# Performance work log

Hardware: AMD Instinct MI355X
Metric: run time of the kernel (lower is better)

## Reference

```python
import jax, jax.numpy as jnp
import numpy as np

B, S, D, L, H = 8, 1024, 512, 6, 8
HD = D // H


def setup_inputs() -> dict:
    key = jax.random.key(0)
    sc = D ** -0.5
    inp = {
        "xr": jax.random.normal(jax.random.fold_in(key, 0), (B, S, D), jnp.float32),
        "xi": jax.random.normal(jax.random.fold_in(key, 1), (B, S, D), jnp.float32),
    }
    wnames = ["Wq_r", "Wq_i", "Wk_r", "Wk_i", "Wv_r", "Wv_i", "Wo_r", "Wo_i",
              "W1_r", "W1_i", "W2_r", "W2_i"]
    for i, n in enumerate(wnames):
        inp[n] = jax.random.normal(jax.random.fold_in(key, 10 + i), (L, D, D), jnp.float32) * sc
    for n in ["bq_r", "bq_i", "bk_r", "bk_i", "bv_r", "bv_i", "bo_r", "bo_i",
              "b1_r", "b1_i", "b2_r", "b2_i"]:
        inp[n] = jnp.zeros((L, D), jnp.float32)
    g0 = 1.0 / np.sqrt(2.0)  # standard complex-LN affine init
    for n in ["ln1_grr", "ln1_gii", "ln2_grr", "ln2_gii"]:
        inp[n] = jnp.full((L, D), g0, jnp.float32)
    for n in ["ln1_gri", "ln1_br", "ln1_bi", "ln2_gri", "ln2_br", "ln2_bi"]:
        inp[n] = jnp.zeros((L, D), jnp.float32)
    return inp


def clin(xr, xi, Wr, Wi, br, bi):
    # ComplexLinear: (xr + i xi)(Wr + i Wi)^T + (br + i bi)
    yr = xr @ Wr.T - xi @ Wi.T + br
    yi = xr @ Wi.T + xi @ Wr.T + bi
    return yr, yi


def cln(xr, xi, grr, gri, gii, br, bi, eps=1e-5):
    # Complex LayerNorm: 2x2 covariance whitening over the feature dim + affine
    mr = xr.mean(-1, keepdims=True)
    mi = xi.mean(-1, keepdims=True)
    cr, ci = xr - mr, xi - mi
    Vrr = (cr * cr).mean(-1, keepdims=True) + eps
    Vii = (ci * ci).mean(-1, keepdims=True) + eps
    Vri = (cr * ci).mean(-1, keepdims=True)
    s = jnp.sqrt(Vrr * Vii - Vri * Vri)
    t = jnp.sqrt(Vrr + Vii + 2.0 * s)
    st = s * t
    Wrr = (Vii + s) / st
    Wii = (Vrr + s) / st
    Wri = -Vri / st
    hr = Wrr * cr + Wri * ci
    hi = Wri * cr + Wii * ci
    return grr * hr + gri * hi + br, gri * hr + gii * hi + bi


def reference(xr, xi,
              Wq_r, Wq_i, bq_r, bq_i, Wk_r, Wk_i, bk_r, bk_i,
              Wv_r, Wv_i, bv_r, bv_i, Wo_r, Wo_i, bo_r, bo_i,
              W1_r, W1_i, b1_r, b1_i, W2_r, W2_i, b2_r, b2_i,
              ln1_grr, ln1_gri, ln1_gii, ln1_br, ln1_bi,
              ln2_grr, ln2_gri, ln2_gii, ln2_br, ln2_bi):
    b, s, d = xr.shape
    nl = Wq_r.shape[0]
    h = H
    hd = d // h
    scale = hd ** -0.5
    for l in range(nl):
        rr, ri = xr, xi
        qr, qi = clin(xr, xi, Wq_r[l], Wq_i[l], bq_r[l], bq_i[l])
        kr, ki = clin(xr, xi, Wk_r[l], Wk_i[l], bk_r[l], bk_i[l])
        vr, vi = clin(xr, xi, Wv_r[l], Wv_i[l], bv_r[l], bv_i[l])
        split = lambda a: a.reshape(b, s, h, hd)
        qr, qi, kr, ki, vr, vi = map(split, (qr, qi, kr, ki, vr, vi))
        # sm_variante='real': softmax over Re(q k^H) = qr.kr + qi.ki
        logits = (jnp.einsum('bqhd,bkhd->bhqk', qr, kr)
                  + jnp.einsum('bqhd,bkhd->bhqk', qi, ki)) * scale
        A = jax.nn.softmax(logits, axis=-1)  # real-valued attention weights
        o_r = jnp.einsum('bhqk,bkhd->bqhd', A, vr).reshape(b, s, d)
        o_i = jnp.einsum('bhqk,bkhd->bqhd', A, vi).reshape(b, s, d)
        o_r, o_i = clin(o_r, o_i, Wo_r[l], Wo_i[l], bo_r[l], bo_i[l])
        xr, xi = o_r + rr, o_i + ri
        xr, xi = cln(xr, xi, ln1_grr[l], ln1_gri[l], ln1_gii[l], ln1_br[l], ln1_bi[l])
        rr, ri = xr, xi
        hr, hi = clin(xr, xi, W1_r[l], W1_i[l], b1_r[l], b1_i[l])
        hr, hi = jax.nn.relu(hr), jax.nn.relu(hi)  # CReLU; dropout = identity (eval)
        hr, hi = clin(hr, hi, W2_r[l], W2_i[l], b2_r[l], b2_i[l])
        xr, xi = hr + rr, hi + ri
        xr, xi = cln(xr, xi, ln2_grr[l], ln2_gri[l], ln2_gii[l], ln2_br[l], ln2_bi[l])
    return jnp.stack([xr, xi])  # [2, B, S, D] (real, imag)
```

## Files before the change

kernel.cpp:

```cpp
#include <hip/hip_runtime.h>
#include <cstddef>
#include <cstdint>

constexpr int NB   = 8;
constexpr int SEQ  = 1024;
constexpr int DIM  = 512;
constexpr int NL   = 6;
constexpr int NH   = 8;
constexpr int HDIM = 64;
constexpr int ROWS = NB * SEQ;
constexpr size_t BSD = (size_t)ROWS * DIM;
constexpr int KHAT = 1024;

typedef __attribute__((ext_vector_type(8))) short bfrag;
typedef __attribute__((ext_vector_type(4))) float f32x4;
typedef __attribute__((ext_vector_type(4))) unsigned short us4;

__device__ __forceinline__ void f4a(const float4 v, float* a) {
    a[0] = v.x; a[1] = v.y; a[2] = v.z; a[3] = v.w;
}
__device__ __forceinline__ float4 a4f(const float* a) {
    float4 v; v.x = a[0]; v.y = a[1]; v.z = a[2]; v.w = a[3]; return v;
}
__device__ __forceinline__ unsigned short f2bf(float f) {
    union { float f; uint32_t u; } x{f};
    return (unsigned short)((x.u + 0x7fffu + ((x.u >> 16) & 1u)) >> 16);
}
__device__ __forceinline__ void gload16(const unsigned short* g, void* l) {
    __builtin_amdgcn_global_load_lds(
        (const __attribute__((address_space(1))) void*)g,
        (__attribute__((address_space(3))) void*)l, 16, 0, 0);
}

struct PrepArgs {
    const float* Wr[6]; const float* Wi[6];
    const float* br[6]; const float* bi[6];
};

__global__ __launch_bounds__(256)
void prep_kernel(PrepArgs a, unsigned short* __restrict__ Ball,
                 float* __restrict__ biasall, int layer)
{
    const int lin = blockIdx.y;
    const int nh_ = blockIdx.x;
    const float* Wr = a.Wr[lin] + (size_t)layer * DIM * DIM;
    const float* Wi = a.Wi[lin] + (size_t)layer * DIM * DIM;

    bool real; int n0;
    if (lin < 3) { const int dh = nh_ & 127; real = dh < 64; n0 = (nh_ >> 7) * 64 + (dh & 63); }
    else         { real = nh_ < 512; n0 = nh_ & 511; }

    const int t = threadIdx.x;
    const int kk = (t * 4) & 511;
    const bool fh = t < 128;
    const float* src;
    float sgn = 1.f;
    if (fh) src = real ? Wr : Wi;
    else { if (real) { src = Wi; sgn = -1.f; } else src = Wr; }

    float v[4];
    f4a(*(const float4*)(src + (size_t)n0 * 512 + kk), v);
    us4 o;
    #pragma unroll
    for (int j = 0; j < 4; ++j) o[j] = f2bf(sgn * v[j]);
    *(us4*)(Ball + (size_t)lin * KHAT * KHAT + (size_t)nh_ * KHAT + t * 4) = o;
    if (t == 0)
        biasall[lin * KHAT + nh_] = real ? a.br[lin][layer * DIM + n0]
                                         : a.bi[lin][layer * DIM + n0];
}

template <int EPI>
__global__ __launch_bounds__(256)
void gemm_mfma(const unsigned short* __restrict__ Xh,
               const unsigned short* __restrict__ Bh,
               const float* __restrict__ bias,
               unsigned short* __restrict__ Yh,
               float* __restrict__ Yr, float* __restrict__ Yi)
{
    __shared__ __align__(16) unsigned short Asm[128 * 32];
    __shared__ __align__(16) unsigned short Bsm[128 * 32];

    const int t = threadIdx.x, lane = t & 63, w = t >> 6;
    const int wm = w >> 1, wn = w & 1;
    const int c = lane & 15, g = lane >> 4;

    int bid = blockIdx.y * 8 + blockIdx.x;
    bid = (bid & 7) * 64 + (bid >> 3);
    const int n0 = (bid & 7) * 128;
    const int m0 = (bid >> 3) * 128;

    f32x4 acc[4][4];
    #pragma unroll
    for (int i = 0; i < 4; ++i)
        #pragma unroll
        for (int j = 0; j < 4; ++j) acc[i][j] = (f32x4){0.f, 0.f, 0.f, 0.f};

    const int srow = (w << 4) + (lane >> 2);
    const int scol = (lane & 3) * 8;
    const unsigned short* gA0 = Xh + (size_t)(m0 + srow) * KHAT + scol;
    const unsigned short* gA1 = Xh + (size_t)(m0 + 64 + srow) * KHAT + scol;
    const unsigned short* gB0 = Bh + (size_t)(n0 + srow) * KHAT + scol;
    const unsigned short* gB1 = Bh + (size_t)(n0 + 64 + srow) * KHAT + scol;
    char* aBase = (char*)Asm + (w << 10);
    char* bBase = (char*)Bsm + (w << 10);

    for (int ks = 0; ks < 32; ++ks) {
        const int k0 = ks * 32;
        __syncthreads();
        gload16(gA0 + k0, aBase);
        gload16(gA1 + k0, aBase + 4096);
        gload16(gB0 + k0, bBase);
        gload16(gB1 + k0, bBase + 4096);
        __syncthreads();

        bfrag af[4], bf2[4];
        #pragma unroll
        for (int mi = 0; mi < 4; ++mi)
            af[mi] = *(const bfrag*)(Asm + (wm * 64 + mi * 16 + c) * 32 + g * 8);
        #pragma unroll
        for (int ni = 0; ni < 4; ++ni)
            bf2[ni] = *(const bfrag*)(Bsm + (wn * 64 + ni * 16 + c) * 32 + g * 8);
        #pragma unroll
        for (int mi = 0; mi < 4; ++mi)
            #pragma unroll
            for (int ni = 0; ni < 4; ++ni)
                acc[mi][ni] = __builtin_amdgcn_mfma_f32_16x16x32_bf16(
                    af[mi], bf2[ni], acc[mi][ni], 0, 0, 0);
    }

    const int mbase = m0 + wm * 64;
    const int nbase = n0 + wn * 64;
    #pragma unroll
    for (int mi = 0; mi < 4; ++mi) {
        #pragma unroll
        for (int ni = 0; ni < 4; ++ni) {
            const int n = nbase + ni * 16 + c;
            const float bv = bias[n];
            float v[4];
            #pragma unroll
            for (int r = 0; r < 4; ++r) v[r] = acc[mi][ni][r] + bv;
            const int mrow = mbase + mi * 16 + g * 4;
            if (EPI == 0) {
                const int b = mrow >> 10, s = mrow & 1023;
                const int h = n >> 7, dh = n & 127;
                const size_t a = ((size_t)(b * NH + h) * SEQ + s) * 128 + dh;
                #pragma unroll
                for (int r = 0; r < 4; ++r) Yh[a + (size_t)r * 128] = f2bf(v[r]);
            } else if (EPI == 1) {
                const int b = mrow >> 10, s = mrow & 1023;
                const int h = n >> 7, dh = n & 127;
                const size_t a = ((size_t)(b * NH + h) * 128 + dh) * SEQ + s;
                us4 o;
                #pragma unroll
                for (int r = 0; r < 4; ++r) o[r] = f2bf(v[r]);
                *(us4*)(Yh + a) = o;
            } else if (EPI == 2) {
                float* dst = (n < 512) ? Yr : Yi;
                const int nn = n & 511;
                #pragma unroll
                for (int r = 0; r < 4; ++r) dst[(size_t)(mrow + r) * DIM + nn] = v[r];
            } else {
                #pragma unroll
                for (int r = 0; r < 4; ++r)
                    Yh[(size_t)(mrow + r) * KHAT + n] = f2bf(fmaxf(v[r], 0.f));
            }
        }
    }
}

__global__ __launch_bounds__(256)
void attn_mfma(const unsigned short* __restrict__ Qh,
               const unsigned short* __restrict__ Kh,
               const unsigned short* __restrict__ Vth,
               unsigned short* __restrict__ Ah)
{
    __shared__ __align__(16) char smem[41216];
    char* Ksm = smem;
    char* Vsm = smem + 16384;
    const int t    = threadIdx.x;
    const int lane = t & 63;
    const int wv   = t >> 6;
    const int c    = lane & 15;
    const int g    = lane >> 4;
    char* Pw = smem + 32768 + wv * 2048;

    int bid = blockIdx.x + 16 * blockIdx.y + 128 * blockIdx.z;
    bid = (bid & 7) * 128 + (bid >> 3);
    const int q0 = (bid & 15) * 64;
    const int bh = bid >> 4;
    const int hh = bh & 7, bb = bh >> 3;
    const size_t qkb = (size_t)bh * SEQ * 128;
    const size_t vtb = (size_t)bh * 128 * SEQ;

    bfrag qf[4];
    {
        const unsigned short* qp = Qh + qkb + (size_t)(q0 + wv * 16 + c) * 128 + g * 8;
        #pragma unroll
        for (int ks = 0; ks < 4; ++ks) qf[ks] = *(const bfrag*)(qp + ks * 32);
    }

    f32x4 oacc[8];
    #pragma unroll
    for (int i = 0; i < 8; ++i) oacc[i] = (f32x4){0.f, 0.f, 0.f, 0.f};
    float mrun[4], lrun[4];
    #pragma unroll
    for (int r = 0; r < 4; ++r) { mrun[r] = -1e30f; lrun[r] = 0.f; }

    const int kkey = t >> 2, kq = t & 3;
    const unsigned short* kgp = Kh + qkb + (size_t)kkey * 128 + kq * 32;
    const int vd = t >> 1, vh2 = t & 1;
    const unsigned short* vgp = Vth + vtb + (size_t)vd * SEQ + vh2 * 32;

    bfrag krg[4], vrg[4];
    #pragma unroll
    for (int j = 0; j < 4; ++j) krg[j] = *(const bfrag*)(kgp + j * 8);
    #pragma unroll
    for (int j = 0; j < 4; ++j) vrg[j] = *(const bfrag*)(vgp + j * 8);

    for (int k0 = 0; k0 < SEQ; k0 += 64) {
        __syncthreads();
        #pragma unroll
        for (int j = 0; j < 4; ++j) {
            const int boff = (kkey * 256 + (kq * 32 + j * 8) * 2) ^ ((kkey & 7) << 4);
            *(bfrag*)(Ksm + boff) = krg[j];
        }
        #pragma unroll
        for (int j = 0; j < 4; ++j) {
            const int boff = (vd * 128 + (vh2 * 32 + j * 8) * 2) ^ ((vd & 7) << 4);
            *(bfrag*)(Vsm + boff) = vrg[j];
        }
        __syncthreads();

        if (k0 + 64 < SEQ) {
            const int kn = k0 + 64;
            #pragma unroll
            for (int j = 0; j < 4; ++j) krg[j] = *(const bfrag*)(kgp + (size_t)kn * 128 + j * 8);
            #pragma unroll
            for (int j = 0; j < 4; ++j) vrg[j] = *(const bfrag*)(vgp + kn + j * 8);
        }

        f32x4 sa[4];
        #pragma unroll
        for (int nt = 0; nt < 4; ++nt) sa[nt] = (f32x4){0.f, 0.f, 0.f, 0.f};
        __builtin_amdgcn_s_setprio(1);
        #pragma unroll
        for (int nt = 0; nt < 4; ++nt) {
            const int key = nt * 16 + c;
            #pragma unroll
            for (int ks = 0; ks < 4; ++ks) {
                const int boff = (key * 256 + (ks * 32 + g * 8) * 2) ^ ((key & 7) << 4);
                const bfrag bk = *(const bfrag*)(Ksm + boff);
                sa[nt] = __builtin_amdgcn_mfma_f32_16x16x32_bf16(qf[ks], bk, sa[nt], 0, 0, 0);
            }
        }
        __builtin_amdgcn_s_setprio(0);

        float sv[4][4];
        #pragma unroll
        for (int nt = 0; nt < 4; ++nt)
            #pragma unroll
            for (int r = 0; r < 4; ++r) sv[nt][r] = sa[nt][r] * 0.125f;

        float mt[4], ps[4], mn[4];
        #pragma unroll
        for (int r = 0; r < 4; ++r)
            mt[r] = fmaxf(fmaxf(sv[0][r], sv[1][r]), fmaxf(sv[2][r], sv[3][r]));
        #pragma unroll
        for (int m = 1; m <= 8; m <<= 1) {
            #pragma unroll
            for (int r = 0; r < 4; ++r) mt[r] = fmaxf(mt[r], __shfl_xor(mt[r], m, 64));
        }
        bool big = false;
        #pragma unroll
        for (int r = 0; r < 4; ++r) big |= (mt[r] > mrun[r] + 8.f);
        const bool refresh = __any(big);
        float fs[4];
        if (refresh) {
            #pragma unroll
            for (int r = 0; r < 4; ++r) {
                mn[r] = fmaxf(mrun[r], mt[r]);
                fs[r] = __expf(mrun[r] - mn[r]);
            }
        } else {
            #pragma unroll
            for (int r = 0; r < 4; ++r) { mn[r] = mrun[r]; fs[r] = 1.f; }
        }
        #pragma unroll
        for (int r = 0; r < 4; ++r) ps[r] = 0.f;

        #pragma unroll
        for (int nt = 0; nt < 4; ++nt) {
            const int col2 = (nt * 16 + c) * 2;
            #pragma unroll
            for (int r = 0; r < 4; ++r) {
                const float p = __expf(sv[nt][r] - mn[r]);
                ps[r] += p;
                const int qrow = 4 * g + r;
                *(unsigned short*)(Pw + ((qrow * 128 + col2) ^ ((qrow & 7) << 4))) = f2bf(p);
            }
        }
        #pragma unroll
        for (int m = 1; m <= 8; m <<= 1) {
            #pragma unroll
            for (int r = 0; r < 4; ++r) ps[r] += __shfl_xor(ps[r], m, 64);
        }
        #pragma unroll
        for (int r = 0; r < 4; ++r) {
            lrun[r] = lrun[r] * fs[r] + ps[r];
            mrun[r] = mn[r];
        }

        if (refresh) {
            const int rr = c & 3;
            float vsel = fs[0];
            vsel = (rr == 1) ? fs[1] : vsel;
            vsel = (rr == 2) ? fs[2] : vsel;
            vsel = (rr == 3) ? fs[3] : vsel;
            const float fsc = __shfl(vsel, ((c >> 2) << 4) | (c & 3), 64);
            #pragma unroll
            for (int i = 0; i < 8; ++i) {
                oacc[i][0] *= fsc; oacc[i][1] *= fsc; oacc[i][2] *= fsc; oacc[i][3] *= fsc;
            }
        }

        asm volatile("s_waitcnt lgkmcnt(0)" ::: "memory");
        __builtin_amdgcn_sched_barrier(0);

        __builtin_amdgcn_s_setprio(1);
        #pragma unroll
        for (int k2 = 0; k2 < 2; ++k2) {
            const int kb2 = (k2 * 32 + g * 8) * 2;
            const bfrag pb = *(const bfrag*)(Pw + ((c * 128 + kb2) ^ ((c & 7) << 4)));
            #pragma unroll
            for (int mtl = 0; mtl < 8; ++mtl) {
                const int d = mtl * 16 + c;
                const bfrag va = *(const bfrag*)(Vsm + ((d * 128 + kb2) ^ ((d & 7) << 4)));
                oacc[mtl] = __builtin_amdgcn_mfma_f32_16x16x32_bf16(va, pb, oacc[mtl], 0, 0, 0);
            }
        }
        __builtin_amdgcn_s_setprio(0);
    }

    {
        const int rr = c & 3;
        float inv[4];
        #pragma unroll
        for (int r = 0; r < 4; ++r) inv[r] = 1.f / lrun[r];
        float vsel = inv[0];
        vsel = (rr == 1) ? inv[1] : vsel;
        vsel = (rr == 2) ? inv[2] : vsel;
        vsel = (rr == 3) ? inv[3] : vsel;
        const float ic = __shfl(vsel, ((c >> 2) << 4) | (c & 3), 64);
        #pragma unroll
        for (int i = 0; i < 8; ++i) {
            oacc[i][0] *= ic; oacc[i][1] *= ic; oacc[i][2] *= ic; oacc[i][3] *= ic;
        }
    }
    __syncthreads();
    float* Ox = (float*)(smem + wv * 8192);
    #pragma unroll
    for (int mtl = 0; mtl < 8; ++mtl)
        #pragma unroll
        for (int r = 0; r < 4; ++r)
            Ox[(mtl * 16 + 4 * g + r) * 16 + c] = oacc[mtl][r];
    asm volatile("s_waitcnt lgkmcnt(0)" ::: "memory");
    __builtin_amdgcn_sched_barrier(0);

    const int q = lane >> 2, qt = lane & 3;
    const int colbase = (qt >> 1) * 512 + hh * 64 + (qt & 1) * 32;
    const size_t rowm = (size_t)bb * SEQ + q0 + wv * 16 + q;
    unsigned short* dst = Ah + rowm * KHAT + colbase;
    #pragma unroll
    for (int j = 0; j < 8; ++j) {
        us4 o;
        #pragma unroll
        for (int e = 0; e < 4; ++e) o[e] = f2bf(Ox[(qt * 32 + j * 4 + e) * 16 + q]);
        *(us4*)(dst + j * 4) = o;
    }
}

__global__ __launch_bounds__(256)
void cln_kernel(const float* __restrict__ Ur, const float* __restrict__ Ui,
                float* __restrict__ Xr, float* __restrict__ Xi,
                unsigned short* __restrict__ Xh,
                const float* __restrict__ Grr, const float* __restrict__ Gri,
                const float* __restrict__ Gii, const float* __restrict__ Bbr,
                const float* __restrict__ Bbi)
{
    const int lane = threadIdx.x & 63;
    const int row  = blockIdx.x * 4 + (threadIdx.x >> 6);
    const size_t off = (size_t)row * DIM;
    const int c0 = lane * 4;
    const int c1 = 256 + lane * 4;

    float xr[8], xi[8];
    {
        float a[4], b[4];
        f4a(*(const float4*)&Ur[off + c0], a); f4a(*(const float4*)&Xr[off + c0], b);
        #pragma unroll
        for (int j = 0; j < 4; ++j) xr[j] = a[j] + b[j];
        f4a(*(const float4*)&Ur[off + c1], a); f4a(*(const float4*)&Xr[off + c1], b);
        #pragma unroll
        for (int j = 0; j < 4; ++j) xr[4 + j] = a[j] + b[j];
        f4a(*(const float4*)&Ui[off + c0], a); f4a(*(const float4*)&Xi[off + c0], b);
        #pragma unroll
        for (int j = 0; j < 4; ++j) xi[j] = a[j] + b[j];
        f4a(*(const float4*)&Ui[off + c1], a); f4a(*(const float4*)&Xi[off + c1], b);
        #pragma unroll
        for (int j = 0; j < 4; ++j) xi[4 + j] = a[j] + b[j];
    }

    float sr = 0.f, si = 0.f, srr = 0.f, sii = 0.f, sri = 0.f;
    #pragma unroll
    for (int j = 0; j < 8; ++j) {
        sr += xr[j]; si += xi[j];
        srr = fmaf(xr[j], xr[j], srr);
        sii = fmaf(xi[j], xi[j], sii);
        sri = fmaf(xr[j], xi[j], sri);
    }
    #pragma unroll
    for (int m = 32; m >= 1; m >>= 1) {
        sr  += __shfl_xor(sr,  m, 64);
        si  += __shfl_xor(si,  m, 64);
        srr += __shfl_xor(srr, m, 64);
        sii += __shfl_xor(sii, m, 64);
        sri += __shfl_xor(sri, m, 64);
    }

    const float inv_d = 1.0f / DIM;
    const float mr = sr * inv_d, mi = si * inv_d;
    const float Vrr = srr * inv_d - mr * mr + 1e-5f;
    const float Vii = sii * inv_d - mi * mi + 1e-5f;
    const float Vri = sri * inv_d - mr * mi;
    const float s  = sqrtf(Vrr * Vii - Vri * Vri);
    const float tt = sqrtf(Vrr + Vii + 2.0f * s);
    const float ist = 1.0f / (s * tt);
    const float Wrr = (Vii + s) * ist;
    const float Wii = (Vrr + s) * ist;
    const float Wri = -Vri * ist;

    #pragma unroll
    for (int half = 0; half < 2; ++half) {
        const int c = half ? c1 : c0;
        float grr[4], gri[4], gii[4], pbr[4], pbi[4];
        f4a(*(const float4*)&Grr[c], grr);
        f4a(*(const float4*)&Gri[c], gri);
        f4a(*(const float4*)&Gii[c], gii);
        f4a(*(const float4*)&Bbr[c], pbr);
        f4a(*(const float4*)&Bbi[c], pbi);
        float outr[4], outi[4];
        #pragma unroll
        for (int j = 0; j < 4; ++j) {
            const int idx = half * 4 + j;
            const float cr = xr[idx] - mr;
            const float ci = xi[idx] - mi;
            const float hr = Wrr * cr + Wri * ci;
            const float hi = Wri * cr + Wii * ci;
            outr[j] = fmaf(grr[j], hr, fmaf(gri[j], hi, pbr[j]));
            outi[j] = fmaf(gri[j], hr, fmaf(gii[j], hi, pbi[j]));
        }
        *(float4*)&Xr[off + c] = a4f(outr);
        *(float4*)&Xi[off + c] = a4f(outi);
        us4 hr_, hi_;
        #pragma unroll
        for (int j = 0; j < 4; ++j) { hr_[j] = f2bf(outr[j]); hi_[j] = f2bf(outi[j]); }
        *(us4*)(Xh + (size_t)row * KHAT + c)       = hr_;
        *(us4*)(Xh + (size_t)row * KHAT + 512 + c) = hi_;
    }
}

__global__ __launch_bounds__(256)
void init_cvt(const float* __restrict__ xr, const float* __restrict__ xi,
              float* __restrict__ outr, float* __restrict__ outi,
              unsigned short* __restrict__ Xh)
{
    const size_t i = ((size_t)blockIdx.x * 256 + threadIdx.x) * 4;
    float vr[4], vi[4];
    f4a(*(const float4*)(xr + i), vr);
    f4a(*(const float4*)(xi + i), vi);
    *(float4*)(outr + i) = a4f(vr);
    *(float4*)(outi + i) = a4f(vi);
    const size_t m = i >> 9;
    const int k = (int)(i & 511);
    us4 a, b;
    #pragma unroll
    for (int j = 0; j < 4; ++j) { a[j] = f2bf(vr[j]); b[j] = f2bf(vi[j]); }
    *(us4*)(Xh + m * KHAT + k)       = a;
    *(us4*)(Xh + m * KHAT + 512 + k) = b;
}

extern "C" void kernel_launch(void* const* d_in, const int* in_sizes, int n_in,
                              void* d_out, int out_size, void* d_ws, size_t ws_size,
                              hipStream_t stream) {
    (void)in_sizes; (void)n_in; (void)out_size; (void)ws_size;

    const float* in_xr = (const float*)d_in[0];
    const float* in_xi = (const float*)d_in[1];
    PrepArgs pa;
    pa.Wr[0] = (const float*)d_in[2];  pa.Wi[0] = (const float*)d_in[3];
    pa.Wr[1] = (const float*)d_in[4];  pa.Wi[1] = (const float*)d_in[5];
    pa.Wr[2] = (const float*)d_in[6];  pa.Wi[2] = (const float*)d_in[7];
    pa.Wr[3] = (const float*)d_in[8];  pa.Wi[3] = (const float*)d_in[9];
    pa.Wr[4] = (const float*)d_in[10]; pa.Wi[4] = (const float*)d_in[11];
    pa.Wr[5] = (const float*)d_in[12]; pa.Wi[5] = (const float*)d_in[13];
    pa.br[0] = (const float*)d_in[14]; pa.bi[0] = (const float*)d_in[15];
    pa.br[1] = (const float*)d_in[16]; pa.bi[1] = (const float*)d_in[17];
    pa.br[2] = (const float*)d_in[18]; pa.bi[2] = (const float*)d_in[19];
    pa.br[3] = (const float*)d_in[20]; pa.bi[3] = (const float*)d_in[21];
    pa.br[4] = (const float*)d_in[22]; pa.bi[4] = (const float*)d_in[23];
    pa.br[5] = (const float*)d_in[24]; pa.bi[5] = (const float*)d_in[25];
    const float* ln1_grr = (const float*)d_in[26];
    const float* ln1_gii = (const float*)d_in[27];
    const float* ln2_grr = (const float*)d_in[28];
    const float* ln2_gii = (const float*)d_in[29];
    const float* ln1_gri = (const float*)d_in[30];
    const float* ln1_br  = (const float*)d_in[31];
    const float* ln1_bi  = (const float*)d_in[32];
    const float* ln2_gri = (const float*)d_in[33];
    const float* ln2_br  = (const float*)d_in[34];
    const float* ln2_bi  = (const float*)d_in[35];

    float* outr = (float*)d_out;
    float* outi = outr + BSD;

    char* ws = (char*)d_ws;
    unsigned short* Xh  = (unsigned short*)(ws);
    unsigned short* Qh  = (unsigned short*)(ws + 16777216);
    unsigned short* Kh  = (unsigned short*)(ws + 2 * 16777216);
    unsigned short* Vth = (unsigned short*)(ws + 3 * 16777216);
    unsigned short* Ah  = (unsigned short*)(ws + 4 * 16777216);
    unsigned short* Ball = (unsigned short*)(ws + 5 * 16777216);
    float* biasall = (float*)(ws + 5 * 16777216 + 12582912);
    float* Pr = (float*)Kh;
    float* Pi = (float*)Vth;
    unsigned short* Hh = Qh;

    init_cvt<<<ROWS * DIM / 1024, 256, 0, stream>>>(in_xr, in_xi, outr, outi, Xh);

    const dim3 pgrid(KHAT, 6);
    const dim3 ggrid(KHAT / 128, ROWS / 128);
    const dim3 agrid(SEQ / 64, NH, NB);
    const int  lgrid = ROWS / 4;

    for (int l = 0; l < NL; ++l) {
        const size_t bo = (size_t)l * DIM;
        prep_kernel<<<pgrid, 256, 0, stream>>>(pa, Ball, biasall, l);

        unsigned short* Bq = Ball;
        unsigned short* Bk = Ball + (size_t)1 * KHAT * KHAT;
        unsigned short* Bv = Ball + (size_t)2 * KHAT * KHAT;
        unsigned short* Bo = Ball + (size_t)3 * KHAT * KHAT;
        unsigned short* B1 = Ball + (size_t)4 * KHAT * KHAT;
        unsigned short* B2 = Ball + (size_t)5 * KHAT * KHAT;

        gemm_mfma<0><<<ggrid, 256, 0, stream>>>(Xh, Bq, biasall + 0 * KHAT, Qh, nullptr, nullptr);
        gemm_mfma<0><<<ggrid, 256, 0, stream>>>(Xh, Bk, biasall + 1 * KHAT, Kh, nullptr, nullptr);
        gemm_mfma<1><<<ggrid, 256, 0, stream>>>(Xh, Bv, biasall + 2 * KHAT, Vth, nullptr, nullptr);
        attn_mfma<<<agrid, 256, 0, stream>>>(Qh, Kh, Vth, Ah);
        gemm_mfma<2><<<ggrid, 256, 0, stream>>>(Ah, Bo, biasall + 3 * KHAT, nullptr, Pr, Pi);
        cln_kernel<<<lgrid, 256, 0, stream>>>(Pr, Pi, outr, outi, Xh,
                                              ln1_grr + bo, ln1_gri + bo, ln1_gii + bo,
                                              ln1_br + bo, ln1_bi + bo);
        gemm_mfma<3><<<ggrid, 256, 0, stream>>>(Xh, B1, biasall + 4 * KHAT, Hh, nullptr, nullptr);
        gemm_mfma<2><<<ggrid, 256, 0, stream>>>(Hh, B2, biasall + 5 * KHAT, nullptr, Pr, Pi);
        cln_kernel<<<lgrid, 256, 0, stream>>>(Pr, Pi, outr, outi, Xh,
                                              ln2_grr + bo, ln2_gri + bo, ln2_gii + bo,
                                              ln2_br + bo, ln2_bi + bo);
    }
}
```

Measured before the change: 1.706 ms.

## Fuse QKV GEMMs, compute softmax rowsum via MFMA, store GEMM outputs as bf16

Merges the three Q/K/V projection GEMMs into one launch with a 24-wide N grid that picks the weight slice and output layout per block. Attention now uses exp2 with a pre-scaled log2e factor and a wider lazy-rescale threshold. It skips the cross-lane max reduction unless a rescale is needed and gets the row sum from an extra MFMA against a ones vector instead of shuffle reductions. The O-projection and FFN2 outputs are written as bf16 instead of fp32 and converted back inside the complex LayerNorm kernel, which halves that traffic but lowers residual-path precision.

```diff
diff --git a/kernel.cpp b/kernel.cpp
--- a/kernel.cpp
+++ b/kernel.cpp
@@ -26,6 +26,11 @@
     union { float f; uint32_t u; } x{f};
     return (unsigned short)((x.u + 0x7fffu + ((x.u >> 16) & 1u)) >> 16);
 }
+__device__ __forceinline__ float bf2f(unsigned short u) {
+    union { uint32_t u; float f; } x;
+    x.u = (uint32_t)u << 16;
+    return x.f;
+}
 __device__ __forceinline__ void gload16(const unsigned short* g, void* l) {
     __builtin_amdgcn_global_load_lds(
         (const __attribute__((address_space(1))) void*)g,
@@ -69,13 +74,13 @@
                                          : a.bi[lin][layer * DIM + n0];
 }
 
-template <int EPI>
 __global__ __launch_bounds__(256)
-void gemm_mfma(const unsigned short* __restrict__ Xh,
-               const unsigned short* __restrict__ Bh,
-               const float* __restrict__ bias,
-               unsigned short* __restrict__ Yh,
-               float* __restrict__ Yr, float* __restrict__ Yi)
+void gemm_qkv(const unsigned short* __restrict__ Xh,
+              const unsigned short* __restrict__ Ball,
+              const float* __restrict__ biasall,
+              unsigned short* __restrict__ Qh,
+              unsigned short* __restrict__ Kh,
+              unsigned short* __restrict__ Vth)
 {
     __shared__ __align__(16) unsigned short Asm[128 * 32];
     __shared__ __align__(16) unsigned short Bsm[128 * 32];
@@ -84,10 +89,15 @@
     const int wm = w >> 1, wn = w & 1;
     const int c = lane & 15, g = lane >> 4;
 
-    int bid = blockIdx.y * 8 + blockIdx.x;
-    bid = (bid & 7) * 64 + (bid >> 3);
-    const int n0 = (bid & 7) * 128;
-    const int m0 = (bid >> 3) * 128;
+    int bid = blockIdx.y * 24 + blockIdx.x;
+    bid = (bid & 7) * 192 + (bid >> 3);
+    const int nblk = bid % 24, mblk = bid / 24;
+    const int n0g = nblk * 128;
+    const int m0 = mblk * 128;
+    const int lin = n0g >> 10;
+    const int n0 = n0g & 1023;
+    const unsigned short* Bh = Ball + (size_t)lin * KHAT * KHAT;
+    const float* bias = biasall + lin * KHAT;
 
     f32x4 acc[4][4];
     #pragma unroll
@@ -130,6 +140,7 @@
 
     const int mbase = m0 + wm * 64;
     const int nbase = n0 + wn * 64;
+    unsigned short* dqk = (lin == 0) ? Qh : Kh;
     #pragma unroll
     for (int mi = 0; mi < 4; ++mi) {
         #pragma unroll
@@ -140,29 +151,95 @@
             #pragma unroll
             for (int r = 0; r < 4; ++r) v[r] = acc[mi][ni][r] + bv;
             const int mrow = mbase + mi * 16 + g * 4;
-            if (EPI == 0) {
-                const int b = mrow >> 10, s = mrow & 1023;
-                const int h = n >> 7, dh = n & 127;
+            const int b = mrow >> 10, s = mrow & 1023;
+            const int h = n >> 7, dh = n & 127;
+            if (lin < 2) {
                 const size_t a = ((size_t)(b * NH + h) * SEQ + s) * 128 + dh;
                 #pragma unroll
-                for (int r = 0; r < 4; ++r) Yh[a + (size_t)r * 128] = f2bf(v[r]);
-            } else if (EPI == 1) {
-                const int b = mrow >> 10, s = mrow & 1023;
-                const int h = n >> 7, dh = n & 127;
+                for (int r = 0; r < 4; ++r) dqk[a + (size_t)r * 128] = f2bf(v[r]);
+            } else {
                 const size_t a = ((size_t)(b * NH + h) * 128 + dh) * SEQ + s;
                 us4 o;
                 #pragma unroll
                 for (int r = 0; r < 4; ++r) o[r] = f2bf(v[r]);
-                *(us4*)(Yh + a) = o;
-            } else if (EPI == 2) {
-                float* dst = (n < 512) ? Yr : Yi;
-                const int nn = n & 511;
-                #pragma unroll
-                for (int r = 0; r < 4; ++r) dst[(size_t)(mrow + r) * DIM + nn] = v[r];
-            } else {
-                #pragma unroll
-                for (int r = 0; r < 4; ++r)
-                    Yh[(size_t)(mrow + r) * KHAT + n] = f2bf(fmaxf(v[r], 0.f));
+                *(us4*)(Vth + a) = o;
+            }
+        }
+    }
+}
+
+template <bool RELU>
+__global__ __launch_bounds__(256)
+void gemm_mfma(const unsigned short* __restrict__ Xh,
+               const unsigned short* __restrict__ Bh,
+               const float* __restrict__ bias,
+               unsigned short* __restrict__ Yh)
+{
+    __shared__ __align__(16) unsigned short Asm[128 * 32];
+    __shared__ __align__(16) unsigned short Bsm[128 * 32];
+
+    const int t = threadIdx.x, lane = t & 63, w = t >> 6;
+    const int wm = w >> 1, wn = w & 1;
+    const int c = lane & 15, g = lane >> 4;
+
+    int bid = blockIdx.y * 8 + blockIdx.x;
+    bid = (bid & 7) * 64 + (bid >> 3);
+    const int n0 = (bid & 7) * 128;
+    const int m0 = (bid >> 3) * 128;
+
+    f32x4 acc[4][4];
+    #pragma unroll
+    for (int i = 0; i < 4; ++i)
+        #pragma unroll
+        for (int j = 0; j < 4; ++j) acc[i][j] = (f32x4){0.f, 0.f, 0.f, 0.f};
+
+    const int srow = (w << 4) + (lane >> 2);
+    const int scol = (lane & 3) * 8;
+    const unsigned short* gA0 = Xh + (size_t)(m0 + srow) * KHAT + scol;
+    const unsigned short* gA1 = Xh + (size_t)(m0 + 64 + srow) * KHAT + scol;
+    const unsigned short* gB0 = Bh + (size_t)(n0 + srow) * KHAT + scol;
+    const unsigned short* gB1 = Bh + (size_t)(n0 + 64 + srow) * KHAT + scol;
+    char* aBase = (char*)Asm + (w << 10);
+    char* bBase = (char*)Bsm + (w << 10);
+
+    for (int ks = 0; ks < 32; ++ks) {
+        const int k0 = ks * 32;
+        __syncthreads();
+        gload16(gA0 + k0, aBase);
+        gload16(gA1 + k0, aBase + 4096);
+        gload16(gB0 + k0, bBase);
+        gload16(gB1 + k0, bBase + 4096);
+        __syncthreads();
+
+        bfrag af[4], bf2[4];
+        #pragma unroll
+        for (int mi = 0; mi < 4; ++mi)
+            af[mi] = *(const bfrag*)(Asm + (wm * 64 + mi * 16 + c) * 32 + g * 8);
+        #pragma unroll
+        for (int ni = 0; ni < 4; ++ni)
+            bf2[ni] = *(const bfrag*)(Bsm + (wn * 64 + ni * 16 + c) * 32 + g * 8);
+        #pragma unroll
+        for (int mi = 0; mi < 4; ++mi)
+            #pragma unroll
+            for (int ni = 0; ni < 4; ++ni)
+                acc[mi][ni] = __builtin_amdgcn_mfma_f32_16x16x32_bf16(
+                    af[mi], bf2[ni], acc[mi][ni], 0, 0, 0);
+    }
+
+    const int mbase = m0 + wm * 64;
+    const int nbase = n0 + wn * 64;
+    #pragma unroll
+    for (int mi = 0; mi < 4; ++mi) {
+        #pragma unroll
+        for (int ni = 0; ni < 4; ++ni) {
+            const int n = nbase + ni * 16 + c;
+            const float bv = bias[n];
+            const int mrow = mbase + mi * 16 + g * 4;
+            #pragma unroll
+            for (int r = 0; r < 4; ++r) {
+                float v = acc[mi][ni][r] + bv;
+                if (RELU) v = fmaxf(v, 0.f);
+                Yh[(size_t)(mrow + r) * KHAT + n] = f2bf(v);
             }
         }
     }
@@ -192,19 +269,26 @@
     const size_t qkb = (size_t)bh * SEQ * 128;
     const size_t vtb = (size_t)bh * 128 * SEQ;
 
+    constexpr float SC  = 0.125f * 1.44269504f;
+    constexpr float THR = 11.0f;
+
     bfrag qf[4];
     {
         const unsigned short* qp = Qh + qkb + (size_t)(q0 + wv * 16 + c) * 128 + g * 8;
         #pragma unroll
         for (int ks = 0; ks < 4; ++ks) qf[ks] = *(const bfrag*)(qp + ks * 32);
     }
+    bfrag vones;
+    #pragma unroll
+    for (int j = 0; j < 8; ++j) vones[j] = (short)0x3F80;
 
     f32x4 oacc[8];
     #pragma unroll
     for (int i = 0; i < 8; ++i) oacc[i] = (f32x4){0.f, 0.f, 0.f, 0.f};
-    float mrun[4], lrun[4];
-    #pragma unroll
-    for (int r = 0; r < 4; ++r) { mrun[r] = -1e30f; lrun[r] = 0.f; }
+    f32x4 oaccl = (f32x4){0.f, 0.f, 0.f, 0.f};
+    float mrun[4];
+    #pragma unroll
+    for (int r = 0; r < 4; ++r) mrun[r] = -1e30f;
 
     const int kkey = t >> 2, kq = t & 3;
     const unsigned short* kgp = Kh + qkb + (size_t)kkey * 128 + kq * 32;
@@ -259,58 +343,30 @@
         #pragma unroll
         for (int nt = 0; nt < 4; ++nt)
             #pragma unroll
-            for (int r = 0; r < 4; ++r) sv[nt][r] = sa[nt][r] * 0.125f;
-
-        float mt[4], ps[4], mn[4];
+            for (int r = 0; r < 4; ++r) sv[nt][r] = sa[nt][r] * SC;
+
+        float mloc[4];
         #pragma unroll
         for (int r = 0; r < 4; ++r)
-            mt[r] = fmaxf(fmaxf(sv[0][r], sv[1][r]), fmaxf(sv[2][r], sv[3][r]));
-        #pragma unroll
-        for (int m = 1; m <= 8; m <<= 1) {
-            #pragma unroll
-            for (int r = 0; r < 4; ++r) mt[r] = fmaxf(mt[r], __shfl_xor(mt[r], m, 64));
-        }
+            mloc[r] = fmaxf(fmaxf(sv[0][r], sv[1][r]), fmaxf(sv[2][r], sv[3][r]));
         bool big = false;
         #pragma unroll
-        for (int r = 0; r < 4; ++r) big |= (mt[r] > mrun[r] + 8.f);
-        const bool refresh = __any(big);
-        float fs[4];
-        if (refresh) {
+        for (int r = 0; r < 4; ++r) big |= (mloc[r] > mrun[r] + THR);
+        if (__any(big)) {
+            float mt[4], fs[4];
+            #pragma unroll
+            for (int r = 0; r < 4; ++r) mt[r] = mloc[r];
+            #pragma unroll
+            for (int m = 1; m <= 8; m <<= 1) {
+                #pragma unroll
+                for (int r = 0; r < 4; ++r) mt[r] = fmaxf(mt[r], __shfl_xor(mt[r], m, 64));
+            }
             #pragma unroll
             for (int r = 0; r < 4; ++r) {
-                mn[r] = fmaxf(mrun[r], mt[r]);
-                fs[r] = __expf(mrun[r] - mn[r]);
-            }
-        } else {
-            #pragma unroll
-            for (int r = 0; r < 4; ++r) { mn[r] = mrun[r]; fs[r] = 1.f; }
-        }
-        #pragma unroll
-        for (int r = 0; r < 4; ++r) ps[r] = 0.f;
-
-        #pragma unroll
-        for (int nt = 0; nt < 4; ++nt) {
-            const int col2 = (nt * 16 + c) * 2;
-            #pragma unroll
-            for (int r = 0; r < 4; ++r) {
-                const float p = __expf(sv[nt][r] - mn[r]);
-                ps[r] += p;
-                const int qrow = 4 * g + r;
-                *(unsigned short*)(Pw + ((qrow * 128 + col2) ^ ((qrow & 7) << 4))) = f2bf(p);
-            }
-        }
-        #pragma unroll
-        for (int m = 1; m <= 8; m <<= 1) {
-            #pragma unroll
-            for (int r = 0; r < 4; ++r) ps[r] += __shfl_xor(ps[r], m, 64);
-        }
-        #pragma unroll
-        for (int r = 0; r < 4; ++r) {
-            lrun[r] = lrun[r] * fs[r] + ps[r];
-            mrun[r] = mn[r];
-        }
-
-        if (refresh) {
+                const float mn = fmaxf(mrun[r], mt[r]);
+                fs[r] = exp2f(mrun[r] - mn);
+                mrun[r] = mn;
+            }
             const int rr = c & 3;
             float vsel = fs[0];
             vsel = (rr == 1) ? fs[1] : vsel;
@@ -321,6 +377,18 @@
             for (int i = 0; i < 8; ++i) {
                 oacc[i][0] *= fsc; oacc[i][1] *= fsc; oacc[i][2] *= fsc; oacc[i][3] *= fsc;
             }
+            oaccl[0] *= fsc; oaccl[1] *= fsc; oaccl[2] *= fsc; oaccl[3] *= fsc;
+        }
+
+        #pragma unroll
+        for (int nt = 0; nt < 4; ++nt) {
+            const int col2 = (nt * 16 + c) * 2;
+            #pragma unroll
+            for (int r = 0; r < 4; ++r) {
+                const float p = exp2f(sv[nt][r] - mrun[r]);
+                const int qrow = 4 * g + r;
+                *(unsigned short*)(Pw + ((qrow * 128 + col2) ^ ((qrow & 7) << 4))) = f2bf(p);
+            }
         }
 
         asm volatile("s_waitcnt lgkmcnt(0)" ::: "memory");
@@ -337,20 +405,13 @@
                 const bfrag va = *(const bfrag*)(Vsm + ((d * 128 + kb2) ^ ((d & 7) << 4)));
                 oacc[mtl] = __builtin_amdgcn_mfma_f32_16x16x32_bf16(va, pb, oacc[mtl], 0, 0, 0);
             }
+            oaccl = __builtin_amdgcn_mfma_f32_16x16x32_bf16(vones, pb, oaccl, 0, 0, 0);
         }
         __builtin_amdgcn_s_setprio(0);
     }
 
     {
-        const int rr = c & 3;
-        float inv[4];
-        #pragma unroll
-        for (int r = 0; r < 4; ++r) inv[r] = 1.f / lrun[r];
-        float vsel = inv[0];
-        vsel = (rr == 1) ? inv[1] : vsel;
-        vsel = (rr == 2) ? inv[2] : vsel;
-        vsel = (rr == 3) ? inv[3] : vsel;
-        const float ic = __shfl(vsel, ((c >> 2) << 4) | (c & 3), 64);
+        const float ic = 1.0f / oaccl[0];
         #pragma unroll
         for (int i = 0; i < 8; ++i) {
             oacc[i][0] *= ic; oacc[i][1] *= ic; oacc[i][2] *= ic; oacc[i][3] *= ic;
@@ -380,7 +441,7 @@
 }
 
 __global__ __launch_bounds__(256)
-void cln_kernel(const float* __restrict__ Ur, const float* __restrict__ Ui,
+void cln_kernel(const unsigned short* __restrict__ U,
                 float* __restrict__ Xr, float* __restrict__ Xi,
                 unsigned short* __restrict__ Xh,
                 const float* __restrict__ Grr, const float* __restrict__ Gri,
@@ -395,19 +456,20 @@
 
     float xr[8], xi[8];
     {
-        float a[4], b[4];
-        f4a(*(const float4*)&Ur[off + c0], a); f4a(*(const float4*)&Xr[off + c0], b);
-        #pragma unroll
-        for (int j = 0; j < 4; ++j) xr[j] = a[j] + b[j];
-        f4a(*(const float4*)&Ur[off + c1], a); f4a(*(const float4*)&Xr[off + c1], b);
-        #pragma unroll
-        for (int j = 0; j < 4; ++j) xr[4 + j] = a[j] + b[j];
-        f4a(*(const float4*)&Ui[off + c0], a); f4a(*(const float4*)&Xi[off + c0], b);
-        #pragma unroll
-        for (int j = 0; j < 4; ++j) xi[j] = a[j] + b[j];
-        f4a(*(const float4*)&Ui[off + c1], a); f4a(*(const float4*)&Xi[off + c1], b);
-        #pragma unroll
-        for (int j = 0; j < 4; ++j) xi[4 + j] = a[j] + b[j];
+        const unsigned short* up = U + (size_t)row * KHAT;
+        us4 a0 = *(const us4*)(up + c0);
+        us4 a1 = *(const us4*)(up + c1);
+        us4 b0 = *(const us4*)(up + 512 + c0);
+        us4 b1 = *(const us4*)(up + 512 + c1);
+        float t0[4], t1[4];
+        f4a(*(const float4*)&Xr[off + c0], t0);
+        f4a(*(const float4*)&Xr[off + c1], t1);
+        #pragma unroll
+        for (int j = 0; j < 4; ++j) { xr[j] = bf2f(a0[j]) + t0[j]; xr[4 + j] = bf2f(a1[j]) + t1[j]; }
+        f4a(*(const float4*)&Xi[off + c0], t0);
+        f4a(*(const float4*)&Xi[off + c1], t1);
+        #pragma unroll
+        for (int j = 0; j < 4; ++j) { xi[j] = bf2f(b0[j]) + t0[j]; xi[4 + j] = bf2f(b1[j]) + t1[j]; }
     }
 
     float sr = 0.f, si = 0.f, srr = 0.f, sii = 0.f, sri = 0.f;
@@ -531,13 +593,13 @@
     unsigned short* Ah  = (unsigned short*)(ws + 4 * 16777216);
     unsigned short* Ball = (unsigned short*)(ws + 5 * 16777216);
     float* biasall = (float*)(ws + 5 * 16777216 + 12582912);
-    float* Pr = (float*)Kh;
-    float* Pi = (float*)Vth;
+    unsigned short* Uh = Kh;
     unsigned short* Hh = Qh;
 
     init_cvt<<<ROWS * DIM / 1024, 256, 0, stream>>>(in_xr, in_xi, outr, outi, Xh);
 
     const dim3 pgrid(KHAT, 6);
+    const dim3 qgrid(24, ROWS / 128);
     const dim3 ggrid(KHAT / 128, ROWS / 128);
     const dim3 agrid(SEQ / 64, NH, NB);
     const int  lgrid = ROWS / 4;
@@ -546,24 +608,19 @@
         const size_t bo = (size_t)l * DIM;
         prep_kernel<<<pgrid, 256, 0, stream>>>(pa, Ball, biasall, l);
 
-        unsigned short* Bq = Ball;
-        unsigned short* Bk = Ball + (size_t)1 * KHAT * KHAT;
-        unsigned short* Bv = Ball + (size_t)2 * KHAT * KHAT;
         unsigned short* Bo = Ball + (size_t)3 * KHAT * KHAT;
         unsigned short* B1 = Ball + (size_t)4 * KHAT * KHAT;
         unsigned short* B2 = Ball + (size_t)5 * KHAT * KHAT;
 
-        gemm_mfma<0><<<ggrid, 256, 0, stream>>>(Xh, Bq, biasall + 0 * KHAT, Qh, nullptr, nullptr);
-        gemm_mfma<0><<<ggrid, 256, 0, stream>>>(Xh, Bk, biasall + 1 * KHAT, Kh, nullptr, nullptr);
-        gemm_mfma<1><<<ggrid, 256, 0, stream>>>(Xh, Bv, biasall + 2 * KHAT, Vth, nullptr, nullptr);
+        gemm_qkv<<<qgrid, 256, 0, stream>>>(Xh, Ball, biasall, Qh, Kh, Vth);
         attn_mfma<<<agrid, 256, 0, stream>>>(Qh, Kh, Vth, Ah);
-        gemm_mfma<2><<<ggrid, 256, 0, stream>>>(Ah, Bo, biasall + 3 * KHAT, nullptr, Pr, Pi);
-        cln_kernel<<<lgrid, 256, 0, stream>>>(Pr, Pi, outr, outi, Xh,
+        gemm_mfma<false><<<ggrid, 256, 0, stream>>>(Ah, Bo, biasall + 3 * KHAT, Uh);
+        cln_kernel<<<lgrid, 256, 0, stream>>>(Uh, outr, outi, Xh,
                                               ln1_grr + bo, ln1_gri + bo, ln1_gii + bo,
                                               ln1_br + bo, ln1_bi + bo);
-        gemm_mfma<3><<<ggrid, 256, 0, stream>>>(Xh, B1, biasall + 4 * KHAT, Hh, nullptr, nullptr);
-        gemm_mfma<2><<<ggrid, 256, 0, stream>>>(Hh, B2, biasall + 5 * KHAT, nullptr, Pr, Pi);
-        cln_kernel<<<lgrid, 256, 0, stream>>>(Pr, Pi, outr, outi, Xh,
+        gemm_mfma<true><<<ggrid, 256, 0, stream>>>(Xh, B1, biasall + 4 * KHAT, Hh);
+        gemm_mfma<false><<<ggrid, 256, 0, stream>>>(Hh, B2, biasall + 5 * KHAT, Uh);
+        cln_kernel<<<lgrid, 256, 0, stream>>>(Uh, outr, outi, Xh,
                                               ln2_grr + bo, ln2_gri + bo, ln2_gii + bo,
                                               ln2_br + bo, ln2_bi + bo);
     }
```

Result: faster. 1.516 ms (-11.2%).
